# Kernel optimization log

Hardware: AMD Instinct MI355X
Metric: run time of the kernel (lower is better)

Reference implementation:

```python
import jax, jax.numpy as jnp
import numpy as np

B, S, D = 8, 2048, 512
E, DF = 16, 2048  # total experts, FFN hidden (4*d_model)
K = 4             # num_available_experts


def setup_inputs() -> dict:
    key = jax.random.key(0)
    ks = jax.random.split(key, 5)
    scale = 0.02
    return {
        "x": jax.random.normal(ks[0], (B, S, D), dtype=jnp.float32),
        "gate_w": jax.random.normal(ks[1], (E, D), dtype=jnp.float32) * scale,
        "gate_b": jnp.zeros((E,), dtype=jnp.float32),
        "w1": jax.random.normal(ks[2], (E, D, DF), dtype=jnp.float32) * scale,
        "b1": jnp.zeros((E, DF), dtype=jnp.float32),
        "w2": jax.random.normal(ks[3], (E, DF, D), dtype=jnp.float32) * scale,
        "b2": jnp.zeros((E, D), dtype=jnp.float32),
        "num_available": K,
    }


def reference(x, gate_w, gate_b, w1, b1, w2, b2, num_available):
    # Coarse expert selection: gate applied to the global token sum k = sum_{b,s} x
    k = jnp.sum(x, axis=(0, 1))                       # [D]
    coarse = gate_w @ k + gate_b                      # [E]
    _, idx = jax.lax.top_k(coarse, num_available)     # [K]

    # Gather selected experts' params
    gw_w, gw_b = gate_w[idx], gate_b[idx]             # [K,D], [K]
    W1, B1 = w1[idx], b1[idx]                         # [K,D,DF], [K,DF]
    W2, B2 = w2[idx], b2[idx]                         # [K,DF,D], [K,D]

    # Per-token softmax gating over the K selected experts
    logits = jnp.einsum('bsd,kd->bsk', x, gw_w) + gw_b  # [B,S,K]
    gw = jax.nn.softmax(logits, axis=2)                 # [B,S,K]

    # Dense expert FFNs over all tokens, weighted combine
    h = jax.nn.gelu(jnp.einsum('bsd,kdf->kbsf', x, W1) + B1[:, None, None, :])  # [K,B,S,DF]
    eo = jnp.einsum('kbsf,kfd->kbsd', h, W2) + B2[:, None, None, :]             # [K,B,S,D]
    out = jnp.einsum('kbsd,bsk->bsd', eo, gw)                                   # [B,S,D]
    return out
```

## Files before the change

kernel.cpp:

```cpp
#include <hip/hip_runtime.h>
#include <hip/hip_bf16.h>
#include <cstdint>
#include <cstddef>

typedef __attribute__((ext_vector_type(8))) short short8;
typedef __attribute__((ext_vector_type(4))) float f32x4;

#define AS1U32(p) ((const __attribute__((address_space(1))) uint32_t*)(p))
#define AS3U32(p) ((__attribute__((address_space(3))) uint32_t*)(p))

__device__ __forceinline__ unsigned short f2bf(float v) {
  union { float f; uint32_t u; } a; a.f = v;
  uint32_t u = a.u;
  u += 0x7FFFu + ((u >> 16) & 1u);
  return (unsigned short)(u >> 16);
}

__device__ __forceinline__ float gelu_fast(float x) {
  const float c0 = 0.7978845608028654f;
  const float c1 = 0.044715f;
  float u = c0 * (x + c1 * x * x * x);
  return x * __builtin_amdgcn_rcpf(1.0f + __expf(-2.0f * u));
}


__global__ __launch_bounds__(512)
void reduce_part(const float* __restrict__ x, float* __restrict__ kpart) {
  const int d = threadIdx.x;
  const int b = blockIdx.x;
  float s = 0.f;
#pragma unroll 4
  for (int i = 0; i < 64; i++)
    s += x[((size_t)b * 64 + i) * 512 + d];
  kpart[(size_t)b * 512 + d] = s;
}

__global__ __launch_bounds__(1024)
void gate_all(const float* __restrict__ kpart,
              const float* __restrict__ gate_w,
              const float* __restrict__ gate_b,
              const float* __restrict__ b1, const float* __restrict__ b2,
              int* __restrict__ idxout,
              float* __restrict__ b1cat, float* __restrict__ b2sel) {
  __shared__ float ksum2[2][512];
  __shared__ float coarse[16];
  __shared__ int idxl[4];
  const int t = threadIdx.x;
  {
    const int d = t & 511, h = t >> 9;
    float s = 0.f;
    for (int p = h * 128; p < h * 128 + 128; p++) s += kpart[(size_t)p * 512 + d];
    ksum2[h][d] = s;
  }
  __syncthreads();
  {
    const int wave = t >> 6, lane = t & 63;
    const int d0 = lane * 8;
    float s = 0.f;
#pragma unroll
    for (int j = 0; j < 8; j++)
      s += gate_w[wave * 512 + d0 + j] * (ksum2[0][d0 + j] + ksum2[1][d0 + j]);
#pragma unroll
    for (int off = 32; off >= 1; off >>= 1) s += __shfl_down(s, off, 64);
    if (lane == 0) coarse[wave] = s + gate_b[wave];
  }
  __syncthreads();
  if (t == 0) {
    unsigned taken = 0;
    for (int r = 0; r < 4; r++) {
      float best = -3.4e38f; int bi = 0;
      for (int e = 0; e < 16; e++)
        if (!((taken >> e) & 1u) && coarse[e] > best) { best = coarse[e]; bi = e; }
      taken |= 1u << bi;
      idxl[r] = bi; idxout[r] = bi;
    }
  }
  __syncthreads();
  for (int i = t; i < 8192; i += 1024)
    b1cat[i] = b1[(size_t)idxl[i >> 11] * 2048 + (i & 2047)];
  for (int i = t; i < 2048; i += 1024)
    b2sel[i] = b2[(size_t)idxl[i >> 9] * 512 + (i & 511)];
}

__global__ __launch_bounds__(256)
void transpose_all(const float* __restrict__ w1, const float* __restrict__ w2,
                   unsigned short* __restrict__ w1t, unsigned short* __restrict__ w2t,
                   const int* __restrict__ idx) {
  __shared__ float tl[64][65];
  const int tid = threadIdx.x;
  const int ty = tid >> 6, tx = tid & 63;
  const int z = blockIdx.z;
  const float* src; unsigned short* dbase; int C, dstLd, r0, c0;
  if (z < 4) {
    src = w1 + (size_t)idx[z] * 512 * 2048;
    dbase = w1t + (size_t)z * 2048 * 512;
    C = 2048; dstLd = 512;
    r0 = blockIdx.x * 64; c0 = blockIdx.y * 64;
  } else {
    src = w2 + (size_t)idx[z - 4] * 2048 * 512;
    dbase = w2t + (size_t)(z - 4) * 2048;
    C = 512; dstLd = 8192;
    r0 = blockIdx.y * 64; c0 = blockIdx.x * 64;
  }
#pragma unroll
  for (int i = 0; i < 16; i++) {
    int r = ty * 16 + i;
    tl[r][tx] = src[(size_t)(r0 + r) * C + c0 + tx];
  }
  __syncthreads();
#pragma unroll
  for (int i = 0; i < 16; i++) {
    int rr = ty * 16 + i;
    dbase[(size_t)(c0 + rr) * dstLd + r0 + tx] = f2bf(tl[tx][rr]);
  }
}

__global__ __launch_bounds__(256)
void gate_softmax_xconv(const float* __restrict__ x,
                        const float* __restrict__ gate_w,
                        const float* __restrict__ gate_b,
                        const int* __restrict__ idx,
                        float* __restrict__ gwout,
                        unsigned short* __restrict__ xbf) {
  __shared__ float wsel[4][512];
  __shared__ float bsel[4];
  const int tid = threadIdx.x;
  for (int i = tid; i < 2048; i += 256) {
    int k = i >> 9;
    wsel[k][i & 511] = gate_w[(size_t)idx[k] * 512 + (i & 511)];
  }
  if (tid < 4) bsel[tid] = gate_b[idx[tid]];
  __syncthreads();
  const int wave = tid >> 6, lane = tid & 63;
  const int t = blockIdx.x * 4 + wave;
  const float* xr = x + (size_t)t * 512 + lane * 8;
  float4 v0 = ((const float4*)xr)[0];
  float4 v1 = ((const float4*)xr)[1];
  float vals[8] = {v0.x, v0.y, v0.z, v0.w, v1.x, v1.y, v1.z, v1.w};
  short8 pk;
#pragma unroll
  for (int j = 0; j < 8; j++) pk[j] = (short)f2bf(vals[j]);
  *(short8*)(xbf + (size_t)t * 512 + lane * 8) = pk;
  float a0 = 0.f, a1 = 0.f, a2 = 0.f, a3 = 0.f;
  const int dbase = lane * 8;
#pragma unroll
  for (int j = 0; j < 8; j++) {
    float xv = vals[j];
    a0 += xv * wsel[0][dbase + j];
    a1 += xv * wsel[1][dbase + j];
    a2 += xv * wsel[2][dbase + j];
    a3 += xv * wsel[3][dbase + j];
  }
#pragma unroll
  for (int off = 32; off >= 1; off >>= 1) {
    a0 += __shfl_down(a0, off, 64);
    a1 += __shfl_down(a1, off, 64);
    a2 += __shfl_down(a2, off, 64);
    a3 += __shfl_down(a3, off, 64);
  }
  if (lane == 0) {
    float l0 = a0 + bsel[0], l1 = a1 + bsel[1], l2 = a2 + bsel[2], l3 = a3 + bsel[3];
    float m = fmaxf(fmaxf(l0, l1), fmaxf(l2, l3));
    float e0 = __expf(l0 - m), e1 = __expf(l1 - m);
    float e2 = __expf(l2 - m), e3 = __expf(l3 - m);
    float inv = 1.0f / (e0 + e1 + e2 + e3);
    float* o = gwout + (size_t)t * 4;
    o[0] = e0 * inv; o[1] = e1 * inv; o[2] = e2 * inv; o[3] = e3 * inv;
  }
}


#define CFENCE asm volatile("" ::: "memory")
#define BAR    do { CFENCE; __builtin_amdgcn_s_barrier(); CFENCE; } while (0)
#define LGKM0  do { asm volatile("s_waitcnt lgkmcnt(0)" ::: "memory"); \
                    __builtin_amdgcn_sched_barrier(0); } while (0)
#define VMW(n) asm volatile("s_waitcnt vmcnt(" #n ")" ::: "memory")

#define LDA(abuf, mh)                                                       \
  do {                                                                      \
    _Pragma("unroll")                                                       \
    for (int m_ = 0; m_ < 4; m_++)                                          \
      _Pragma("unroll")                                                     \
      for (int ks_ = 0; ks_ < 2; ks_++)                                     \
        aF[m_][ks_] = *(const short8*)((abuf) +                             \
            (size_t)(wr * 128 + ((mh) * 4 + m_) * 16 + fr) * 64 +           \
            (((ks_ * 4 + quad) ^ swz) * 8));                                \
  } while (0)

#define LDB(bbuf, nh)                                                       \
  do {                                                                      \
    _Pragma("unroll")                                                       \
    for (int n_ = 0; n_ < NF2; n_++)                                        \
      _Pragma("unroll")                                                     \
      for (int ks_ = 0; ks_ < 2; ks_++)                                     \
        bF[nh][n_][ks_] = *(const short8*)((bbuf) +                         \
            (size_t)(wc * NWV + ((nh) * NF2 + n_) * 16 + fr) * 64 +         \
            (((ks_ * 4 + quad) ^ swz) * 8));                                \
  } while (0)

#define MM(mh, nh)                                                          \
  do {                                                                      \
    __builtin_amdgcn_s_setprio(1);                                          \
    _Pragma("unroll")                                                       \
    for (int m_ = 0; m_ < 4; m_++)                                          \
      _Pragma("unroll")                                                     \
      for (int n_ = 0; n_ < NF2; n_++)                                      \
        _Pragma("unroll")                                                   \
        for (int ks_ = 0; ks_ < 2; ks_++)                                   \
          acc[(mh) * 4 + m_][(nh) * NF2 + n_] =                             \
              __builtin_amdgcn_mfma_f32_16x16x32_bf16(                      \
                  aF[m_][ks_], bF[nh][n_][ks_],                             \
                  acc[(mh) * 4 + m_][(nh) * NF2 + n_], 0, 0, 0);            \
    __builtin_amdgcn_s_setprio(0);                                          \
  } while (0)

template <int NFREP, int EPI>
__global__ __launch_bounds__(512, 2)
void gemm8p(const unsigned short* __restrict__ A,
            const unsigned short* __restrict__ Bt,
            void* __restrict__ C, int K, int lda, int ldb, int ldc,
            const float* __restrict__ gw,
            const float* __restrict__ bias, int colOff, int accum, int doswz) {
  constexpr int BM = 256;
  constexpr int BN = NFREP * 64;
  constexpr int NWV = NFREP * 16;
  constexpr int NF2 = NFREP / 2;
  __shared__ unsigned short lds[2 * (BM * 64 + BN * 64)];

  const int tid = threadIdx.x;
  const int wave = tid >> 6, lane = tid & 63;
  const int lrow = lane >> 3, lslot = lane & 7, gch = lslot ^ lrow;
  const int wr = wave >> 2, wc = wave & 3;
  const int fr = lane & 15, quad = lane >> 4, swz = fr & 7;

  int bx = blockIdx.x, by = blockIdx.y;
  if (doswz) {
    int nwg = gridDim.x * gridDim.y;
    int lin = by * gridDim.x + bx;
    int sw = (lin & 7) * (nwg >> 3) + (lin >> 3);
    bx = sw % gridDim.x; by = sw / gridDim.x;
  }
  const int rowA0 = bx * BM;
  const int rowB0 = by * BN;

  unsigned short* const A0 = lds;
  unsigned short* const B0 = lds + BM * 64;
  unsigned short* const A1 = lds + (BM * 64 + BN * 64);
  unsigned short* const B1 = A1 + BM * 64;

  auto stA = [&](unsigned short* ab, int h, int kt) {
#pragma unroll
    for (int j = 0; j < 2; j++) {
      int rg = h * 8 + wave + j * 16;
      const unsigned short* gp =
          A + (size_t)(rowA0 + rg * 8 + lrow) * lda + kt + gch * 8;
      __builtin_amdgcn_global_load_lds(AS1U32(gp), AS3U32(ab + rg * 512), 16, 0, 0);
    }
  };
  auto stB = [&](unsigned short* bb, int nh, int kt) {
    if constexpr (NFREP == 4) {
#pragma unroll
      for (int j = 0; j < 2; j++) {
        int idx = j * 8 + wave;
        int rg = (idx >> 2) * 8 + (idx & 3) + nh * 4;
        const unsigned short* gp =
            Bt + (size_t)(rowB0 + rg * 8 + lrow) * ldb + kt + gch * 8;
        __builtin_amdgcn_global_load_lds(AS1U32(gp), AS3U32(bb + rg * 512), 16, 0, 0);
      }
    } else {
      int rg = (wave >> 1) * 4 + (wave & 1) + nh * 2;
      const unsigned short* gp =
          Bt + (size_t)(rowB0 + rg * 8 + lrow) * ldb + kt + gch * 8;
      __builtin_amdgcn_global_load_lds(AS1U32(gp), AS3U32(bb + rg * 512), 16, 0, 0);
    }
  };

  f32x4 acc[8][NFREP];
#pragma unroll
  for (int i = 0; i < 8; i++)
#pragma unroll
    for (int j = 0; j < NFREP; j++) acc[i][j] = (f32x4){0.f, 0.f, 0.f, 0.f};

  short8 aF[4][2];
  short8 bF[2][NF2][2];

  stB(B0, 0, 0); stB(B0, 1, 0); stA(A0, 0, 0); stA(A0, 1, 0);
  stB(B1, 0, 64); stB(B1, 1, 64); stA(A1, 0, 64); stA(A1, 1, 64);
  if constexpr (NFREP == 4) VMW(8); else VMW(6);
  BAR;

  const int niter = K >> 7;
  for (int i = 0; i < niter - 1; i++) {
    const int kt = i * 128;
    LDA(A0, 0); LDB(B0, 0);
    BAR; LGKM0; MM(0, 0); BAR;
    LDB(B0, 1); stB(B0, 0, kt + 128);
    BAR; LGKM0; MM(0, 1); BAR;
    LDA(A0, 1); stB(B0, 1, kt + 128);
    BAR; LGKM0; MM(1, 1); BAR;
    stA(A0, 0, kt + 128);
    BAR; LGKM0; MM(1, 0);
    if constexpr (NFREP == 4) VMW(6); else VMW(4);
    BAR;
    LDA(A1, 0); LDB(B1, 0); stA(A0, 1, kt + 128);
    BAR; LGKM0; MM(0, 0); BAR;
    LDB(B1, 1); stB(B1, 0, kt + 192);
    BAR; LGKM0; MM(0, 1); BAR;
    LDA(A1, 1); stB(B1, 1, kt + 192);
    BAR; LGKM0; MM(1, 1); BAR;
    stA(A1, 0, kt + 192); stA(A1, 1, kt + 192);
    BAR; LGKM0; MM(1, 0);
    if constexpr (NFREP == 4) VMW(8); else VMW(6);
    BAR;
  }
  LDA(A0, 0); LDB(B0, 0); BAR; LGKM0; MM(0, 0); BAR;
  LDB(B0, 1);             BAR; LGKM0; MM(0, 1); BAR;
  LDA(A0, 1);             BAR; LGKM0; MM(1, 1); BAR;
                          BAR; LGKM0; MM(1, 0); VMW(0); BAR;
  LDA(A1, 0); LDB(B1, 0); BAR; LGKM0; MM(0, 0); BAR;
  LDB(B1, 1);             BAR; LGKM0; MM(0, 1); BAR;
  LDA(A1, 1);             BAR; LGKM0; MM(1, 1); BAR;
                          BAR; LGKM0; MM(1, 0);

  if (EPI == 1) {
    unsigned short* Cb = (unsigned short*)C;
    const int kexp = (colOff + rowB0) >> 11;
#pragma unroll
    for (int m = 0; m < 8; m++) {
#pragma unroll
      for (int reg = 0; reg < 4; reg++) {
        int r = rowA0 + wr * 128 + m * 16 + quad * 4 + reg;
        float g = gw[(size_t)r * 4 + kexp];
#pragma unroll
        for (int n = 0; n < NFREP; n++) {
          int col = rowB0 + wc * NWV + n * 16 + fr;
          float v = acc[m][n][reg] + bias[colOff + col];
          Cb[(size_t)r * ldc + col] = f2bf(gelu_fast(v) * g);
        }
      }
    }
  } else {
    float* Cf = (float*)C;
#pragma unroll
    for (int m = 0; m < 8; m++) {
#pragma unroll
      for (int reg = 0; reg < 4; reg++) {
        int r = rowA0 + wr * 128 + m * 16 + quad * 4 + reg;
        size_t t4 = (size_t)r * 4;
        float g0 = gw[t4], g1 = gw[t4 + 1], g2 = gw[t4 + 2], g3 = gw[t4 + 3];
#pragma unroll
        for (int n = 0; n < NFREP; n++) {
          int col = rowB0 + wc * NWV + n * 16 + fr;
          size_t ci = (size_t)r * 512 + col;
          float v = acc[m][n][reg];
          if (accum) v += Cf[ci];
          else v += g0 * bias[col] + g1 * bias[512 + col] +
                    g2 * bias[1024 + col] + g3 * bias[1536 + col];
          Cf[ci] = v;
        }
      }
    }
  }
}

#undef LDA
#undef LDB
#undef MM


extern "C" void kernel_launch(void* const* d_in, const int* in_sizes, int n_in,
                              void* d_out, int out_size, void* d_ws, size_t ws_size,
                              hipStream_t stream) {
  (void)in_sizes; (void)n_in; (void)out_size;
  const float* x      = (const float*)d_in[0];
  const float* gate_w = (const float*)d_in[1];
  const float* gate_b = (const float*)d_in[2];
  const float* w1     = (const float*)d_in[3];
  const float* b1     = (const float*)d_in[4];
  const float* w2     = (const float*)d_in[5];
  const float* b2     = (const float*)d_in[6];

  char* ws = (char*)d_ws;
  int*            idx   = (int*)(ws + 0);
  float*          gw    = (float*)(ws + 4096);
  float*          b1cat = (float*)(ws + 266240);
  float*          b2sel = (float*)(ws + 299008);
  float*          kpart = (float*)(ws + 307200);
  unsigned short* xbf   = (unsigned short*)(ws + 831488);
  unsigned short* w1t   = (unsigned short*)(ws + 17608704);
  unsigned short* w2t   = (unsigned short*)(ws + 25997312);
  unsigned short* hbuf  = (unsigned short*)(ws + 34385920);
  const size_t HBUF_OFF = 34385920;

  size_t avail = ws_size > HBUF_OFF ? ws_size - HBUF_OFF : 0;
  int nslab = 1;
  while (nslab < 16 && (size_t)16384 * (8192 / nslab) * 2 > avail) nslab <<= 1;
  const int slabDF = 8192 / nslab;

  reduce_part<<<256, 512, 0, stream>>>(x, kpart);
  gate_all<<<1, 1024, 0, stream>>>(kpart, gate_w, gate_b, b1, b2, idx, b1cat, b2sel);
  transpose_all<<<dim3(8, 32, 8), 256, 0, stream>>>(w1, w2, w1t, w2t, idx);
  gate_softmax_xconv<<<4096, 256, 0, stream>>>(x, gate_w, gate_b, idx, gw, xbf);

  for (int s = 0; s < nslab; s++) {
    const int c0 = s * slabDF;
    gemm8p<4, 1><<<dim3(64, slabDF / 256), 512, 0, stream>>>(
        xbf, w1t + (size_t)c0 * 512, hbuf,
        512, 512, 512, slabDF,
        gw, b1cat, c0, 0, 0);
    gemm8p<2, 2><<<dim3(64, 4), 512, 0, stream>>>(
        hbuf, w2t + c0, (float*)d_out,
        slabDF, slabDF, 8192, 512,
        gw, b2sel, 0, s > 0, 1);
  }
}
```

Measured before the change: 559.3 us.

## Replace first FFN GEMM with simpler 128x128-tile single-buffered bf16 MFMA kernel

```diff
diff --git a/kernel.cpp b/kernel.cpp
--- a/kernel.cpp
+++ b/kernel.cpp
@@ -166,6 +166,111 @@
     float inv = 1.0f / (e0 + e1 + e2 + e3);
     float* o = gwout + (size_t)t * 4;
     o[0] = e0 * inv; o[1] = e1 * inv; o[2] = e2 * inv; o[3] = e3 * inv;
+  }
+}
+
+template <int EPI>
+__global__ __launch_bounds__(256, 2)
+void gemm_bt(const unsigned short* __restrict__ A,
+             const unsigned short* __restrict__ Bt,
+             void* __restrict__ C, int K, int lda, int ldb, int ldc,
+             const float* __restrict__ gw,
+             const float* __restrict__ bias, int colOff, int accum) {
+  __shared__ unsigned short lA[128 * 64];
+  __shared__ unsigned short lB[128 * 64];
+  const int tid = threadIdx.x;
+  const int wave = tid >> 6;
+  const int lane = tid & 63;
+  const int rowA0 = blockIdx.x * 128;
+  const int rowB0 = blockIdx.y * 128;
+
+  f32x4 acc[4][4];
+#pragma unroll
+  for (int i = 0; i < 4; i++)
+#pragma unroll
+    for (int j = 0; j < 4; j++) acc[i][j] = (f32x4){0.f, 0.f, 0.f, 0.f};
+
+  const int lrow = lane >> 3;
+  const int lslot = lane & 7;
+  const int gchunk = lslot ^ lrow;
+  const int fr = lane & 15;
+  const int quad = lane >> 4;
+  const int wm = (wave >> 1) * 64;
+  const int wn = (wave & 1) * 64;
+  const int swz = fr & 7;
+
+  for (int kt = 0; kt < K; kt += 64) {
+#pragma unroll
+    for (int c = 0; c < 4; c++) {
+      int r = wave * 32 + c * 8 + lrow;
+      const unsigned short* gp = A + (size_t)(rowA0 + r) * lda + kt + gchunk * 8;
+      __builtin_amdgcn_global_load_lds(AS1U32(gp), AS3U32(lA + (wave * 32 + c * 8) * 64), 16, 0, 0);
+    }
+#pragma unroll
+    for (int c = 0; c < 4; c++) {
+      int r = wave * 32 + c * 8 + lrow;
+      const unsigned short* gp = Bt + (size_t)(rowB0 + r) * ldb + kt + gchunk * 8;
+      __builtin_amdgcn_global_load_lds(AS1U32(gp), AS3U32(lB + (wave * 32 + c * 8) * 64), 16, 0, 0);
+    }
+    __syncthreads();
+#pragma unroll
+    for (int ks = 0; ks < 2; ks++) {
+      short8 af[4], bfr[4];
+      const int c = ks * 4 + quad;
+      const int slot = (c ^ swz) << 3;
+#pragma unroll
+      for (int i = 0; i < 4; i++)
+        af[i] = *(const short8*)(lA + (wm + i * 16 + fr) * 64 + slot);
+#pragma unroll
+      for (int j = 0; j < 4; j++)
+        bfr[j] = *(const short8*)(lB + (wn + j * 16 + fr) * 64 + slot);
+#pragma unroll
+      for (int i = 0; i < 4; i++)
+#pragma unroll
+        for (int j = 0; j < 4; j++)
+          acc[i][j] = __builtin_amdgcn_mfma_f32_16x16x32_bf16(af[i], bfr[j], acc[i][j], 0, 0, 0);
+    }
+    __syncthreads();
+  }
+
+  if (EPI == 1) {
+    unsigned short* Cb = (unsigned short*)C;
+    const int kexp = (colOff + rowB0) >> 11;
+#pragma unroll
+    for (int i = 0; i < 4; i++) {
+#pragma unroll
+      for (int reg = 0; reg < 4; reg++) {
+        int r = rowA0 + wm + i * 16 + quad * 4 + reg;
+        float g = gw[(size_t)r * 4 + kexp];
+#pragma unroll
+        for (int j = 0; j < 4; j++) {
+          int n = rowB0 + wn + j * 16 + fr;
+          float v = acc[i][j][reg] + bias[colOff + n];
+          Cb[(size_t)r * ldc + n] = f2bf(gelu_fast(v) * g);
+        }
+      }
+    }
+  } else {
+    float* Cf = (float*)C;
+#pragma unroll
+    for (int i = 0; i < 4; i++) {
+#pragma unroll
+      for (int reg = 0; reg < 4; reg++) {
+        int r = rowA0 + wm + i * 16 + quad * 4 + reg;
+        size_t t4 = (size_t)r * 4;
+        float g0 = gw[t4], g1 = gw[t4 + 1], g2 = gw[t4 + 2], g3 = gw[t4 + 3];
+#pragma unroll
+        for (int j = 0; j < 4; j++) {
+          int n = rowB0 + wn + j * 16 + fr;
+          size_t ci = (size_t)r * 512 + n;
+          float v = acc[i][j][reg];
+          if (accum) v += Cf[ci];
+          else v += g0 * bias[n] + g1 * bias[512 + n] +
+                    g2 * bias[1024 + n] + g3 * bias[1536 + n];
+          Cf[ci] = v;
+        }
+      }
+    }
   }
 }
 
@@ -404,10 +509,10 @@
 
   for (int s = 0; s < nslab; s++) {
     const int c0 = s * slabDF;
-    gemm8p<4, 1><<<dim3(64, slabDF / 256), 512, 0, stream>>>(
+    gemm_bt<1><<<dim3(128, slabDF / 128), 256, 0, stream>>>(
         xbf, w1t + (size_t)c0 * 512, hbuf,
         512, 512, 512, slabDF,
-        gw, b1cat, c0, 0, 0);
+        gw, b1cat, c0, 0);
     gemm8p<2, 2><<<dim3(64, 4), 512, 0, stream>>>(
         hbuf, w2t + c0, (float*)d_out,
         slabDF, slabDF, 8192, 512,
```

Measured after the change: 553.3 us. About the same (-1.1%).
